# Kernel optimization log

Hardware: AMD Instinct MI355X
Metric: run time of the kernel (lower is better)

Reference implementation:

```python
import jax, jax.numpy as jnp
import numpy as np

B, T, N, F_IN = 8, 16, 1000, 16
E = 16000
H, D = 4, 32          # heads, gat_hidden_shape
HL = 64               # lstm hidden
OUT = 8
NEG_SLOPE = 0.2       # PyG GATConv default


def setup_inputs() -> dict:
    key = jax.random.key(0)
    ks = jax.random.split(key, 10)
    def init(k, shape, fan):
        return (jax.random.normal(k, shape, jnp.float32) / np.sqrt(fan)).astype(jnp.float32)
    x = jax.random.normal(ks[0], (B, T, N, F_IN), jnp.float32)
    edge_index = jax.random.randint(ks[1], (2, E), 0, N)
    W_gat = init(ks[2], (F_IN, H * D), F_IN)       # GATConv lin weight
    att_src = init(ks[3], (H, D), D)
    att_dst = init(ks[4], (H, D), D)
    b_gat = jnp.zeros((H * D,), jnp.float32)
    W_ih = init(ks[5], (4 * HL, H * D), H * D)     # LSTM, gate order i,f,g,o
    W_hh = init(ks[6], (4 * HL, HL), HL)
    b_ih = jnp.zeros((4 * HL,), jnp.float32)
    b_hh = jnp.zeros((4 * HL,), jnp.float32)
    W_clf = init(ks[7], (OUT, HL), HL)
    b_clf = jnp.zeros((OUT,), jnp.float32)
    return {"x": x, "edge_index": edge_index, "W_gat": W_gat, "att_src": att_src,
            "att_dst": att_dst, "b_gat": b_gat, "W_ih": W_ih, "W_hh": W_hh,
            "b_ih": b_ih, "b_hh": b_hh, "W_clf": W_clf, "b_clf": b_clf}


def reference(x, edge_index, W_gat, att_src, att_dst, b_gat,
              W_ih, W_hh, b_ih, b_hh, W_clf, b_clf):
    Bx, Tx, Nx, Fx = x.shape
    x_flat = x.reshape(Bx * Tx, Nx, Fx)
    # PyG GATConv adds self-loops by default
    loop = jnp.arange(Nx)
    src = jnp.concatenate([edge_index[0], loop])
    dst = jnp.concatenate([edge_index[1], loop])

    def gat_graph(xg):  # xg: [N, F]
        xp = (xg @ W_gat).reshape(Nx, H, D)                 # [N,H,D]
        a_s = jnp.einsum('nhd,hd->nh', xp, att_src)         # [N,H]
        a_d = jnp.einsum('nhd,hd->nh', xp, att_dst)
        e = jax.nn.leaky_relu(a_s[src] + a_d[dst], NEG_SLOPE)  # [E+N,H]
        m = jax.ops.segment_max(e, dst, num_segments=Nx)       # per-target softmax
        ex = jnp.exp(e - m[dst])
        denom = jax.ops.segment_sum(ex, dst, num_segments=Nx)
        alpha = ex / denom[dst]                                # [E+N,H]
        out = jax.ops.segment_sum(alpha[..., None] * xp[src], dst, num_segments=Nx)
        return out.reshape(Nx, H * D) + b_gat                  # [N, H*D]

    gat = jax.vmap(gat_graph)(x_flat)          # [B*T, N, H*D]
    gat = jax.nn.relu(gat)
    pooled = gat.max(axis=1)                   # global_max_pool -> [B*T, H*D]
    seq = pooled.reshape(Bx, Tx, H * D)

    h0 = jnp.zeros((Bx, HL), jnp.float32)
    c0 = jnp.zeros((Bx, HL), jnp.float32)

    def step(carry, xt):  # xt: [B, H*D]
        h, c = carry
        gates = xt @ W_ih.T + h @ W_hh.T + b_ih + b_hh
        i, f, g, o = jnp.split(gates, 4, axis=-1)
        i, f, o = jax.nn.sigmoid(i), jax.nn.sigmoid(f), jax.nn.sigmoid(o)
        g = jnp.tanh(g)
        c = f * c + i * g
        h = o * jnp.tanh(c)
        return (h, c), None

    (hT, _), _ = jax.lax.scan(step, (h0, c0), seq.transpose(1, 0, 2))
    return hT @ W_clf.T + b_clf                # [B, OUT]
```

## Files before the change

kernel.cpp:

```cpp
#include <hip/hip_runtime.h>
#include <hip/hip_bf16.h>
#include <stdint.h>

namespace {
constexpr int kB = 8, kT = 16, kN = 1000, kF = 16;
constexpr int kE = 16000;
constexpr int kH = 4, kHD = 128;
constexpr int kHL = 64, kOUT = 8;
constexpr int kG = kB * kT;
constexpr float kNeg = 0.2f;
constexpr int kNB = 25;

constexpr size_t CX_WG   = 0;
constexpr size_t CX_ATS  = CX_WG   + 2048;
constexpr size_t CX_ATD  = CX_ATS  + 128;
constexpr size_t CX_BG   = CX_ATD  + 128;
constexpr size_t CX_WIH  = CX_BG   + 128;
constexpr size_t CX_WHH  = CX_WIH  + 32768;
constexpr size_t CX_BIH  = CX_WHH  + 16384;
constexpr size_t CX_BHH  = CX_BIH  + 256;
constexpr size_t CX_WCLF = CX_BHH  + 256;
constexpr size_t CX_BCLF = CX_WCLF + 512;
constexpr size_t CX_TOTAL = CX_BCLF + 8;

constexpr size_t OFF_FLAG  = 0;
constexpr size_t OFF_ROW   = 256;
constexpr size_t OFF_COL   = 4352;
constexpr size_t OFF_POOL  = 68608;
constexpr size_t OFF_CANON = 134400;
constexpr size_t OFF_AS    = 239872;
constexpr size_t OFF_PPART = OFF_AS + (size_t)kG * 288000;
constexpr size_t PPART_BYTES = (size_t)kG * kNB * kHD * 4;

constexpr int kSetupBlocks = 10;
}

__device__ __forceinline__ float bf2f(unsigned short u) {
    return __uint_as_float(((uint32_t)u) << 16);
}
__device__ __forceinline__ float blo(uint32_t u) { return __uint_as_float(u << 16); }
__device__ __forceinline__ unsigned short f2bf(float f) {
    uint32_t u = __float_as_uint(f);
    uint32_t r = (u + 0x7fff + ((u >> 16) & 1)) >> 16;
    return (unsigned short)r;
}
__device__ __forceinline__ float sigm(float x) { return 1.f / (1.f + __expf(-x)); }

__device__ __forceinline__ int detect_isf(const unsigned short* xs, int t,
                                          int nthr, int* sh_cnt) {
    if (t == 0) *sh_cnt = 0;
    __syncthreads();
    int loc = 0;
    for (int i = t; i < 2048; i += nthr) {
        unsigned short u = xs[i];
        int ex = (u >> 7) & 0xff;
        if (u == 0 || (ex >= 97 && ex <= 143)) loc++;
    }
    atomicAdd(sh_cnt, loc);
    __syncthreads();
    return (*sh_cnt >= (2048 * 8) / 10) ? 0 : 1;
}

struct ConvArgs {
    const unsigned short* src[10];
    int n[10];
};

__global__ __launch_bounds__(256) void mega_setup(
        const void* __restrict__ xraw, const int* __restrict__ ei,
        ConvArgs ca,
        const unsigned short* __restrict__ WgR,
        const unsigned short* __restrict__ atsR,
        const unsigned short* __restrict__ atdR,
        int* __restrict__ flag, int* __restrict__ row, int* __restrict__ col,
        unsigned short* __restrict__ canon,
        unsigned short* __restrict__ xp_all,
        float* __restrict__ as_all, float* __restrict__ ad_all,
        unsigned int* __restrict__ pooled) {
    const int t = threadIdx.x;
    const unsigned short* xs = (const unsigned short*)xraw;

    if (blockIdx.x == 0) {
        __shared__ int cnt[1024];
        __shared__ int wtot[4];
        const int lane = t & 63, w = t >> 6;
        for (int i = t; i < 1024; i += 256) cnt[i] = 0;
        __syncthreads();
        const int* dst = ei + kE;
        for (int e = t; e < kE; e += 256) atomicAdd(&cnt[dst[e]], 1);
        __syncthreads();
        const int n0 = 4 * t;
        int c0 = cnt[n0], c1 = cnt[n0 + 1], c2 = cnt[n0 + 2], c3 = cnt[n0 + 3];
        int s0 = c0, s1 = s0 + c1, s2 = s1 + c2, s3 = s2 + c3;
        int tot = s3;
#pragma unroll
        for (int sft = 1; sft < 64; sft <<= 1) {
            int v = __shfl_up(tot, sft, 64);
            if (lane >= sft) tot += v;
        }
        if (lane == 63) wtot[w] = tot;
        __syncthreads();
        int wexcl = 0;
        for (int j = 0; j < w; ++j) wexcl += wtot[j];
        const int excl = wexcl + tot - s3;
        if (t == 0) row[0] = 0;
        if (n0 < kN) {
            row[n0 + 1] = excl + s0;
            row[n0 + 2] = excl + s1;
            row[n0 + 3] = excl + s2;
            row[n0 + 4] = excl + s3;
        }
        __syncthreads();
        cnt[n0] = excl; cnt[n0 + 1] = excl + s0;
        cnt[n0 + 2] = excl + s1; cnt[n0 + 3] = excl + s2;
        __syncthreads();
        for (int e = t; e < kE; e += 256) {
            int d0 = dst[e];
            int pos = atomicAdd(&cnt[d0], 1);
            col[pos] = ei[e];
        }
    } else if (blockIdx.x <= 8) {
        __shared__ int dcnt;
        const int isf = detect_isf(xs, t, 256, &dcnt);
        if (blockIdx.x == 1 && t == 0) *flag = isf;
        const int gid = (int)(blockIdx.x - 1) * 256 + t;
        size_t base = 0;
        for (int s = 0; s < 10; ++s) {
            const int n = ca.n[s];
            if (isf) {
                const float* fp = (const float*)ca.src[s];
                for (int i = gid; i < n; i += 2048) canon[base + i] = f2bf(fp[i]);
            } else {
                const unsigned short* sp = ca.src[s];
                for (int i = gid; i < n; i += 2048) canon[base + i] = sp[i];
            }
            base += (size_t)n;
        }
    } else if (blockIdx.x == 9) {
        for (int i = t; i < kG * kHD; i += 256) pooled[i] = 0u;
    } else {
        __shared__ int dcnt;
        __shared__ float Wl[kF * kHD];
        __shared__ float asl[kHD], adl[kHD];
        __shared__ float xr[64][20];
        __shared__ float ws2[2][4][16];
        const int isf = detect_isf(xs, t, 256, &dcnt);
        const int i0 = blockIdx.x - kSetupBlocks;
        const int v = i0 & 7;
        const int jj = i0 >> 3;
        const int gl = v + 8 * (jj >> 4);
        const int nb = jj & 15;
        if (isf) {
            const float* wf = (const float*)WgR;
            for (int i = t; i < kF * kHD; i += 256) Wl[i] = wf[i];
            if (t < kHD) asl[t] = ((const float*)atsR)[t];
            else if (t < 2 * kHD) adl[t - kHD] = ((const float*)atdR)[t - kHD];
        } else {
            for (int i = t; i < kF * kHD; i += 256) Wl[i] = bf2f(WgR[i]);
            if (t < kHD) asl[t] = bf2f(atsR[t]);
            else if (t < 2 * kHD) adl[t - kHD] = bf2f(atdR[t - kHD]);
        }
        const int n0 = nb * 64;
        const int nn = min(64, kN - n0);
        const size_t xbase = (size_t)gl * kN * kF + (size_t)n0 * kF;
        if (isf) {
            const float* xf = (const float*)xraw;
            for (int i = t; i < nn * kF; i += 256) xr[i >> 4][i & 15] = xf[xbase + i];
        } else {
            for (int i = t; i < nn * kF; i += 256) xr[i >> 4][i & 15] = bf2f(xs[xbase + i]);
        }
        __syncthreads();

        if (t < 128) {
            const int sd = t >> 6, h = (t >> 4) & 3, f = t & 15;
            const float* att = sd ? adl : asl;
            const int d0r = t & 31;
            float acc = 0.f;
#pragma unroll
            for (int i = 0; i < 32; ++i) {
                const int d = (d0r + i) & 31;
                acc += Wl[f * kHD + h * 32 + d] * att[h * 32 + d];
            }
            ws2[sd][h][f] = acc;
        }

        uint32_t* xp32 = (uint32_t*)(xp_all + (size_t)gl * kN * kHD);
        {
            const int p = t & 63;
            const int q = t >> 6;
            const int c0 = 2 * p;
            float wA[kF], wB[kF];
#pragma unroll
            for (int f = 0; f < kF; ++f) {
                wA[f] = Wl[f * kHD + c0];
                wB[f] = Wl[f * kHD + c0 + 1];
            }
            for (int ln = q; ln < nn; ln += 4) {
                const float4* xrv = (const float4*)xr[ln];
                const float4 x0 = xrv[0], x1 = xrv[1], x2 = xrv[2], x3 = xrv[3];
                float vA = x0.x * wA[0]  + x0.y * wA[1]  + x0.z * wA[2]  + x0.w * wA[3]
                         + x1.x * wA[4]  + x1.y * wA[5]  + x1.z * wA[6]  + x1.w * wA[7]
                         + x2.x * wA[8]  + x2.y * wA[9]  + x2.z * wA[10] + x2.w * wA[11]
                         + x3.x * wA[12] + x3.y * wA[13] + x3.z * wA[14] + x3.w * wA[15];
                float vB = x0.x * wB[0]  + x0.y * wB[1]  + x0.z * wB[2]  + x0.w * wB[3]
                         + x1.x * wB[4]  + x1.y * wB[5]  + x1.z * wB[6]  + x1.w * wB[7]
                         + x2.x * wB[8]  + x2.y * wB[9]  + x2.z * wB[10] + x2.w * wB[11]
                         + x3.x * wB[12] + x3.y * wB[13] + x3.z * wB[14] + x3.w * wB[15];
                const uint32_t pk = (uint32_t)f2bf(vA) | ((uint32_t)f2bf(vB) << 16);
                xp32[(size_t)(n0 + ln) * 64 + p] = pk;
            }
        }
        __syncthreads();

        {
            const int n = t >> 2, h = t & 3;
            if (n < nn) {
                const float* xv = xr[n];
                const float* wsv = ws2[0][h];
                const float* wdv = ws2[1][h];
                float accS = 0.f, accD = 0.f;
#pragma unroll
                for (int f = 0; f < kF; ++f) {
                    const float xf = xv[f];
                    accS += xf * wsv[f];
                    accD += xf * wdv[f];
                }
                as_all[((size_t)gl * kN + n0 + n) * kH + h] = accS;
                ad_all[((size_t)gl * kN + n0 + n) * kH + h] = accD;
            }
        }
    }
}

__global__ __launch_bounds__(256) void gat_aggregate(
        const int* __restrict__ row, const int* __restrict__ col,
        const unsigned short* __restrict__ xp,
        const float* __restrict__ a_s, const float* __restrict__ a_d,
        const unsigned short* __restrict__ bg,
        unsigned int* __restrict__ pooled,
        float* __restrict__ part, int use_part) {
    __shared__ int   col_lds[4][64];
    __shared__ float p_lds[4][4][72];
    __shared__ float pm[4][kHD];

    const int w = threadIdx.x >> 6;
    const int lane = threadIdx.x & 63;
    const int sub = lane >> 4;
    const int cl = lane & 15;
    const int hh = cl >> 2;
    const int xcd = blockIdx.x & 7;
    const int j = blockIdx.x >> 3;
    const int gl = xcd + 8 * (j / kNB);
    const int blk = j % kNB;
    const size_t gn = (size_t)gl * kN;
    const char* xpcl = (const char*)(xp + gn * kHD) + cl * 16;
    const float4* as4 = (const float4*)a_s + gn;
    const float4* ad4 = (const float4*)a_d + gn;
    const uint32_t* bg32 = (const uint32_t*)bg;
    float bgv[8];
#pragma unroll
    for (int jb = 0; jb < 4; ++jb) {
        uint32_t u = bg32[cl * 4 + jb];
        bgv[2 * jb] = blo(u);
        bgv[2 * jb + 1] = __uint_as_float(u & 0xffff0000u);
    }
    float pool[8];
#pragma unroll
    for (int jb = 0; jb < 8; ++jb) pool[jb] = 0.f;

    for (int it = 0; it < 10; ++it) {
        const int n = blk * 40 + it * 4 + w;
        const int r0 = row[n];
        const int deg = row[n + 1] - r0;
        const int E = deg + 1;
        const float4 dv = ad4[n];
        float acc[8];
#pragma unroll
        for (int jb = 0; jb < 8; ++jb) acc[jb] = 0.f;
        float dh = 0.f;

        for (int base = 0; base < E; base += 64) {
            const int cnt = min(64, E - base);
            const int cntP = (cnt + 3) & ~3;
            if (lane < cntP) {
                const int eg = base + lane;
                const bool act = lane < cnt;
                const int s = (act && eg < deg) ? col[r0 + eg] : n;
                float p0 = 0.f, p1 = 0.f, p2 = 0.f, p3 = 0.f;
                if (act) {
                    const float4 av = as4[s];
                    float t0 = av.x + dv.x, t1 = av.y + dv.y;
                    float t2 = av.z + dv.z, t3 = av.w + dv.w;
                    t0 = t0 > 0.f ? t0 : kNeg * t0;
                    t1 = t1 > 0.f ? t1 : kNeg * t1;
                    t2 = t2 > 0.f ? t2 : kNeg * t2;
                    t3 = t3 > 0.f ? t3 : kNeg * t3;
                    p0 = __expf(t0); p1 = __expf(t1);
                    p2 = __expf(t2); p3 = __expf(t3);
                }
                col_lds[w][lane] = s << 8;
                p_lds[w][0][lane] = p0;
                p_lds[w][1][lane] = p1;
                p_lds[w][2][lane] = p2;
                p_lds[w][3][lane] = p3;
            }
            for (int e0 = 0; e0 < cntP; e0 += 4) {
                const int e = e0 + sub;
                const int off = col_lds[w][e];
                const float al = p_lds[w][hh][e];
                const uint4 u = *(const uint4*)(xpcl + off);
                acc[0] += al * blo(u.x); acc[1] += al * __uint_as_float(u.x);
                acc[2] += al * blo(u.y); acc[3] += al * __uint_as_float(u.y);
                acc[4] += al * blo(u.z); acc[5] += al * __uint_as_float(u.z);
                acc[6] += al * blo(u.w); acc[7] += al * __uint_as_float(u.w);
                dh += al;
            }
        }
#pragma unroll
        for (int jb = 0; jb < 8; ++jb) {
            acc[jb] += __shfl_xor(acc[jb], 16, 64);
            acc[jb] += __shfl_xor(acc[jb], 32, 64);
        }
        dh += __shfl_xor(dh, 16, 64);
        dh += __shfl_xor(dh, 32, 64);
        const float inv = 1.f / dh;
#pragma unroll
        for (int jb = 0; jb < 8; ++jb) {
            const float o = acc[jb] * inv + bgv[jb];
            pool[jb] = fmaxf(pool[jb], o > 0.f ? o : 0.f);
        }
    }
    if (sub == 0) {
#pragma unroll
        for (int jb = 0; jb < 8; ++jb) pm[w][cl * 8 + jb] = pool[jb];
    }
    __syncthreads();
    if (w == 0 && sub == 0) {
        if (use_part) {
            float* dst = part + ((size_t)gl * kNB + blk) * kHD;
#pragma unroll
            for (int jb = 0; jb < 8; ++jb) {
                const int c = cl * 8 + jb;
                dst[c] = fmaxf(fmaxf(pm[0][c], pm[1][c]), fmaxf(pm[2][c], pm[3][c]));
            }
        } else {
            const size_t gp = (size_t)gl * kHD;
#pragma unroll
            for (int jb = 0; jb < 8; ++jb) {
                const int c = cl * 8 + jb;
                float vmax = fmaxf(fmaxf(pm[0][c], pm[1][c]), fmaxf(pm[2][c], pm[3][c]));
                atomicMax(pooled + gp + c, __float_as_uint(vmax));
            }
        }
    }
}

__global__ __launch_bounds__(256) void lstm_head(
        const float* __restrict__ pooled, const float* __restrict__ part,
        int use_part,
        const unsigned short* __restrict__ Wih,
        const unsigned short* __restrict__ Whh,
        const unsigned short* __restrict__ bih,
        const unsigned short* __restrict__ bhh,
        const unsigned short* __restrict__ Wclf,
        const unsigned short* __restrict__ bclf,
        const int* __restrict__ flag,
        void* __restrict__ out) {
    const int b = blockIdx.x;
    const int r = threadIdx.x;
    __shared__ float xt[kHD];
    __shared__ float hs[kHL];
    __shared__ float gates[4 * kHL];

    uint32_t wih[64];
    const uint32_t* pw = (const uint32_t*)(Wih + (size_t)r * kHD);
#pragma unroll
    for (int j = 0; j < 64; ++j) wih[j] = pw[j];
    uint32_t whh[32];
    const uint32_t* ph = (const uint32_t*)(Whh + (size_t)r * kHL);
#pragma unroll
    for (int j = 0; j < 32; ++j) whh[j] = ph[j];
    const float bias = bf2f(bih[r]) + bf2f(bhh[r]);

    float c_st = 0.f;
    if (r < kHL) hs[r] = 0.f;
    __syncthreads();

    for (int t = 0; t < kT; ++t) {
        const size_t g = (size_t)b * kT + t;
        if (r < kHD) {
            if (use_part) {
                const float* ps = part + g * kNB * kHD + r;
                float v = ps[0];
#pragma unroll
                for (int k = 1; k < kNB; ++k) v = fmaxf(v, ps[(size_t)k * kHD]);
                xt[r] = v;
            } else {
                xt[r] = pooled[g * kHD + r];
            }
        }
        __syncthreads();
        float a0 = 0.f, a1 = 0.f, a2 = 0.f, a3 = 0.f;
#pragma unroll
        for (int j = 0; j < 64; j += 4) {
            uint32_t u0 = wih[j], u1 = wih[j + 1], u2 = wih[j + 2], u3 = wih[j + 3];
            a0 += blo(u0) * xt[2 * j + 0] + __uint_as_float(u0 & 0xffff0000u) * xt[2 * j + 1];
            a1 += blo(u1) * xt[2 * j + 2] + __uint_as_float(u1 & 0xffff0000u) * xt[2 * j + 3];
            a2 += blo(u2) * xt[2 * j + 4] + __uint_as_float(u2 & 0xffff0000u) * xt[2 * j + 5];
            a3 += blo(u3) * xt[2 * j + 6] + __uint_as_float(u3 & 0xffff0000u) * xt[2 * j + 7];
        }
#pragma unroll
        for (int j = 0; j < 32; j += 4) {
            uint32_t u0 = whh[j], u1 = whh[j + 1], u2 = whh[j + 2], u3 = whh[j + 3];
            a0 += blo(u0) * hs[2 * j + 0] + __uint_as_float(u0 & 0xffff0000u) * hs[2 * j + 1];
            a1 += blo(u1) * hs[2 * j + 2] + __uint_as_float(u1 & 0xffff0000u) * hs[2 * j + 3];
            a2 += blo(u2) * hs[2 * j + 4] + __uint_as_float(u2 & 0xffff0000u) * hs[2 * j + 5];
            a3 += blo(u3) * hs[2 * j + 6] + __uint_as_float(u3 & 0xffff0000u) * hs[2 * j + 7];
        }
        gates[r] = bias + (a0 + a1) + (a2 + a3);
        __syncthreads();
        if (r < kHL) {
            const float iv = sigm(gates[r]);
            const float fv = sigm(gates[kHL + r]);
            const float gv = tanhf(gates[2 * kHL + r]);
            const float ov = sigm(gates[3 * kHL + r]);
            c_st = fv * c_st + iv * gv;
            hs[r] = ov * tanhf(c_st);
        }
        __syncthreads();
    }
    if (r < kOUT) {
        float acc = bf2f(bclf[r]);
#pragma unroll
        for (int k = 0; k < kHL; ++k) acc += hs[k] * bf2f(Wclf[r * kHL + k]);
        if (*flag) ((float*)out)[b * kOUT + r] = acc;
        else ((__hip_bfloat16*)out)[b * kOUT + r] = __float2bfloat16(acc);
    }
}

extern "C" void kernel_launch(void* const* d_in, const int* in_sizes, int n_in,
                              void* d_out, int out_size, void* d_ws, size_t ws_size,
                              hipStream_t stream) {
    const int* ei = (const int*)d_in[1];

    char* ws = (char*)d_ws;
    int*            flag   = (int*)(ws + OFF_FLAG);
    int*            row    = (int*)(ws + OFF_ROW);
    int*            colv   = (int*)(ws + OFF_COL);
    unsigned int*   pooled = (unsigned int*)(ws + OFF_POOL);
    unsigned short* canon  = (unsigned short*)(ws + OFF_CANON);

    unsigned short* cBg   = canon + CX_BG;
    unsigned short* cWih  = canon + CX_WIH;
    unsigned short* cWhh  = canon + CX_WHH;
    unsigned short* cBih  = canon + CX_BIH;
    unsigned short* cBhh  = canon + CX_BHH;
    unsigned short* cWclf = canon + CX_WCLF;
    unsigned short* cBclf = canon + CX_BCLF;

    float*          a_s = (float*)(ws + OFF_AS);
    float*          a_d = (float*)(ws + OFF_AS + (size_t)kG * 16000);
    unsigned short* xp  = (unsigned short*)(ws + OFF_AS + (size_t)kG * 32000);

    const int use_part = (ws_size >= OFF_PPART + PPART_BYTES) ? 1 : 0;
    float* part = (float*)(ws + OFF_PPART);

    ConvArgs ca;
    const int sizes[10] = {2048, 128, 128, 128, 32768, 16384, 256, 256, 512, 8};
    const int which[10] = {2, 3, 4, 5, 6, 7, 8, 9, 10, 11};
    for (int i = 0; i < 10; ++i) {
        ca.src[i] = (const unsigned short*)d_in[which[i]];
        ca.n[i] = sizes[i];
    }

    mega_setup<<<kSetupBlocks + kG * 16, 256, 0, stream>>>(
        d_in[0], ei, ca,
        (const unsigned short*)d_in[2], (const unsigned short*)d_in[3],
        (const unsigned short*)d_in[4],
        flag, row, colv, canon, xp, a_s, a_d, pooled);
    gat_aggregate<<<kG * kNB, 256, 0, stream>>>(row, colv, xp, a_s, a_d, cBg,
                                                pooled, part, use_part);
    lstm_head<<<kB, 256, 0, stream>>>((const float*)pooled, part, use_part,
                                      cWih, cWhh, cBih, cBhh,
                                      cWclf, cBclf, flag, d_out);
}
```

Measured before the change: 223.5 us.

## Restructure GAT projection to per-wave node loops and unroll aggregation by two

The node projection no longer stages weights and features in shared memory per block. Each wavefront keeps its weight columns in registers, walks 32 consecutive nodes, and computes the attention logits with a cross-lane shuffle reduction, which removes the shared-memory staging and the block barriers. The aggregate kernel now uses 16 node-blocks of 63 nodes, packs the column offset and attention weight into one float2 LDS entry, and processes two edges per iteration to raise memory-level parallelism. The dtype-detection sample is also shrunk to 512 elements, which makes the format heuristic more fragile.

```diff
diff --git a/kernel.cpp b/kernel.cpp
--- a/kernel.cpp
+++ b/kernel.cpp
@@ -9,7 +9,9 @@
 constexpr int kHL = 64, kOUT = 8;
 constexpr int kG = kB * kT;
 constexpr float kNeg = 0.2f;
-constexpr int kNB = 25;
+constexpr int kNB = 16;
+constexpr int kNPB = 63;
+constexpr int kPre = 1024;
 
 constexpr size_t CX_WG   = 0;
 constexpr size_t CX_ATS  = CX_WG   + 2048;
@@ -39,6 +41,7 @@
     return __uint_as_float(((uint32_t)u) << 16);
 }
 __device__ __forceinline__ float blo(uint32_t u) { return __uint_as_float(u << 16); }
+__device__ __forceinline__ float bhi(uint32_t u) { return __uint_as_float(u & 0xffff0000u); }
 __device__ __forceinline__ unsigned short f2bf(float f) {
     uint32_t u = __float_as_uint(f);
     uint32_t r = (u + 0x7fff + ((u >> 16) & 1)) >> 16;
@@ -51,14 +54,14 @@
     if (t == 0) *sh_cnt = 0;
     __syncthreads();
     int loc = 0;
-    for (int i = t; i < 2048; i += nthr) {
+    for (int i = t; i < 512; i += nthr) {
         unsigned short u = xs[i];
         int ex = (u >> 7) & 0xff;
         if (u == 0 || (ex >= 97 && ex <= 143)) loc++;
     }
     atomicAdd(sh_cnt, loc);
     __syncthreads();
-    return (*sh_cnt >= (2048 * 8) / 10) ? 0 : 1;
+    return (*sh_cnt >= 410) ? 0 : 1;
 }
 
 struct ConvArgs {
@@ -140,93 +143,78 @@
         for (int i = t; i < kG * kHD; i += 256) pooled[i] = 0u;
     } else {
         __shared__ int dcnt;
-        __shared__ float Wl[kF * kHD];
-        __shared__ float asl[kHD], adl[kHD];
-        __shared__ float xr[64][20];
-        __shared__ float ws2[2][4][16];
         const int isf = detect_isf(xs, t, 256, &dcnt);
-        const int i0 = blockIdx.x - kSetupBlocks;
-        const int v = i0 & 7;
-        const int jj = i0 >> 3;
-        const int gl = v + 8 * (jj >> 4);
-        const int nb = jj & 15;
+        const int lane = t & 63;
+        const int wv = t >> 6;
+        const int wid = (int)(blockIdx.x - kSetupBlocks) * 4 + wv;
+
+        float wA[kF], wB[kF];
+        float as0, as1, ad0, ad1;
         if (isf) {
             const float* wf = (const float*)WgR;
-            for (int i = t; i < kF * kHD; i += 256) Wl[i] = wf[i];
-            if (t < kHD) asl[t] = ((const float*)atsR)[t];
-            else if (t < 2 * kHD) adl[t - kHD] = ((const float*)atdR)[t - kHD];
+#pragma unroll
+            for (int f = 0; f < kF; ++f) {
+                const float2 wp = ((const float2*)(wf + (size_t)f * kHD))[lane];
+                wA[f] = wp.x; wB[f] = wp.y;
+            }
+            const float2 sv = ((const float2*)atsR)[lane];
+            as0 = sv.x; as1 = sv.y;
+            const float2 dv2 = ((const float2*)atdR)[lane];
+            ad0 = dv2.x; ad1 = dv2.y;
         } else {
-            for (int i = t; i < kF * kHD; i += 256) Wl[i] = bf2f(WgR[i]);
-            if (t < kHD) asl[t] = bf2f(atsR[t]);
-            else if (t < 2 * kHD) adl[t - kHD] = bf2f(atdR[t - kHD]);
-        }
-        const int n0 = nb * 64;
-        const int nn = min(64, kN - n0);
-        const size_t xbase = (size_t)gl * kN * kF + (size_t)n0 * kF;
-        if (isf) {
-            const float* xf = (const float*)xraw;
-            for (int i = t; i < nn * kF; i += 256) xr[i >> 4][i & 15] = xf[xbase + i];
-        } else {
-            for (int i = t; i < nn * kF; i += 256) xr[i >> 4][i & 15] = bf2f(xs[xbase + i]);
-        }
-        __syncthreads();
-
-        if (t < 128) {
-            const int sd = t >> 6, h = (t >> 4) & 3, f = t & 15;
-            const float* att = sd ? adl : asl;
-            const int d0r = t & 31;
-            float acc = 0.f;
-#pragma unroll
-            for (int i = 0; i < 32; ++i) {
-                const int d = (d0r + i) & 31;
-                acc += Wl[f * kHD + h * 32 + d] * att[h * 32 + d];
-            }
-            ws2[sd][h][f] = acc;
-        }
-
-        uint32_t* xp32 = (uint32_t*)(xp_all + (size_t)gl * kN * kHD);
-        {
-            const int p = t & 63;
-            const int q = t >> 6;
-            const int c0 = 2 * p;
-            float wA[kF], wB[kF];
+            const uint32_t* w32 = (const uint32_t*)WgR;
 #pragma unroll
             for (int f = 0; f < kF; ++f) {
-                wA[f] = Wl[f * kHD + c0];
-                wB[f] = Wl[f * kHD + c0 + 1];
-            }
-            for (int ln = q; ln < nn; ln += 4) {
-                const float4* xrv = (const float4*)xr[ln];
-                const float4 x0 = xrv[0], x1 = xrv[1], x2 = xrv[2], x3 = xrv[3];
-                float vA = x0.x * wA[0]  + x0.y * wA[1]  + x0.z * wA[2]  + x0.w * wA[3]
-                         + x1.x * wA[4]  + x1.y * wA[5]  + x1.z * wA[6]  + x1.w * wA[7]
-                         + x2.x * wA[8]  + x2.y * wA[9]  + x2.z * wA[10] + x2.w * wA[11]
-                         + x3.x * wA[12] + x3.y * wA[13] + x3.z * wA[14] + x3.w * wA[15];
-                float vB = x0.x * wB[0]  + x0.y * wB[1]  + x0.z * wB[2]  + x0.w * wB[3]
-                         + x1.x * wB[4]  + x1.y * wB[5]  + x1.z * wB[6]  + x1.w * wB[7]
-                         + x2.x * wB[8]  + x2.y * wB[9]  + x2.z * wB[10] + x2.w * wB[11]
-                         + x3.x * wB[12] + x3.y * wB[13] + x3.z * wB[14] + x3.w * wB[15];
-                const uint32_t pk = (uint32_t)f2bf(vA) | ((uint32_t)f2bf(vB) << 16);
-                xp32[(size_t)(n0 + ln) * 64 + p] = pk;
-            }
-        }
-        __syncthreads();
-
-        {
-            const int n = t >> 2, h = t & 3;
-            if (n < nn) {
-                const float* xv = xr[n];
-                const float* wsv = ws2[0][h];
-                const float* wdv = ws2[1][h];
-                float accS = 0.f, accD = 0.f;
-#pragma unroll
-                for (int f = 0; f < kF; ++f) {
-                    const float xf = xv[f];
-                    accS += xf * wsv[f];
-                    accD += xf * wdv[f];
-                }
-                as_all[((size_t)gl * kN + n0 + n) * kH + h] = accS;
-                ad_all[((size_t)gl * kN + n0 + n) * kH + h] = accD;
+                const uint32_t u = w32[f * 64 + lane];
+                wA[f] = blo(u); wB[f] = bhi(u);
+            }
+            const uint32_t us = ((const uint32_t*)atsR)[lane];
+            as0 = blo(us); as1 = bhi(us);
+            const uint32_t ud = ((const uint32_t*)atdR)[lane];
+            ad0 = blo(ud); ad1 = bhi(ud);
+        }
+
+        uint32_t* xp32 = (uint32_t*)xp_all;
+        const int nEnd = min(wid * 32 + 32, kG * kN);
+        for (int node = wid * 32; node < nEnd; ++node) {
+            float xv[kF];
+            if (isf) {
+                const float4* xr4 = (const float4*)((const float*)xraw + (size_t)node * kF);
+                const float4 x0 = xr4[0], x1 = xr4[1], x2 = xr4[2], x3 = xr4[3];
+                xv[0] = x0.x; xv[1] = x0.y; xv[2]  = x0.z; xv[3]  = x0.w;
+                xv[4] = x1.x; xv[5] = x1.y; xv[6]  = x1.z; xv[7]  = x1.w;
+                xv[8] = x2.x; xv[9] = x2.y; xv[10] = x2.z; xv[11] = x2.w;
+                xv[12] = x3.x; xv[13] = x3.y; xv[14] = x3.z; xv[15] = x3.w;
+            } else {
+                const uint4* xr4 = (const uint4*)(xs + (size_t)node * kF);
+                const uint4 q0 = xr4[0], q1 = xr4[1];
+                xv[0]  = blo(q0.x); xv[1]  = bhi(q0.x);
+                xv[2]  = blo(q0.y); xv[3]  = bhi(q0.y);
+                xv[4]  = blo(q0.z); xv[5]  = bhi(q0.z);
+                xv[6]  = blo(q0.w); xv[7]  = bhi(q0.w);
+                xv[8]  = blo(q1.x); xv[9]  = bhi(q1.x);
+                xv[10] = blo(q1.y); xv[11] = bhi(q1.y);
+                xv[12] = blo(q1.z); xv[13] = bhi(q1.z);
+                xv[14] = blo(q1.w); xv[15] = bhi(q1.w);
+            }
+            float vA = 0.f, vB = 0.f;
+#pragma unroll
+            for (int f = 0; f < kF; ++f) {
+                vA = fmaf(xv[f], wA[f], vA);
+                vB = fmaf(xv[f], wB[f], vB);
+            }
+            xp32[(size_t)node * 64 + lane] =
+                (uint32_t)f2bf(vA) | ((uint32_t)f2bf(vB) << 16);
+            float aS = vA * as0 + vB * as1;
+            float aD = vA * ad0 + vB * ad1;
+#pragma unroll
+            for (int sft = 1; sft < 16; sft <<= 1) {
+                aS += __shfl_xor(aS, sft, 64);
+                aD += __shfl_xor(aD, sft, 64);
+            }
+            if ((lane & 15) == 0) {
+                as_all[(size_t)node * kH + (lane >> 4)] = aS;
+                ad_all[(size_t)node * kH + (lane >> 4)] = aD;
             }
         }
     }
@@ -239,8 +227,7 @@
         const unsigned short* __restrict__ bg,
         unsigned int* __restrict__ pooled,
         float* __restrict__ part, int use_part) {
-    __shared__ int   col_lds[4][64];
-    __shared__ float p_lds[4][4][72];
+    __shared__ float2 colal[4][4][66];
     __shared__ float pm[4][kHD];
 
     const int w = threadIdx.x >> 6;
@@ -262,14 +249,16 @@
     for (int jb = 0; jb < 4; ++jb) {
         uint32_t u = bg32[cl * 4 + jb];
         bgv[2 * jb] = blo(u);
-        bgv[2 * jb + 1] = __uint_as_float(u & 0xffff0000u);
+        bgv[2 * jb + 1] = bhi(u);
     }
     float pool[8];
 #pragma unroll
     for (int jb = 0; jb < 8; ++jb) pool[jb] = 0.f;
 
-    for (int it = 0; it < 10; ++it) {
-        const int n = blk * 40 + it * 4 + w;
+    for (int it = 0; it < 16; ++it) {
+        const int lidx = it * 4 + w;
+        const int n = blk * kNPB + lidx;
+        if (lidx >= kNPB || n >= kN) continue;
         const int r0 = row[n];
         const int deg = row[n + 1] - r0;
         const int E = deg + 1;
@@ -281,7 +270,7 @@
 
         for (int base = 0; base < E; base += 64) {
             const int cnt = min(64, E - base);
-            const int cntP = (cnt + 3) & ~3;
+            const int cntP = (cnt + 7) & ~7;
             if (lane < cntP) {
                 const int eg = base + lane;
                 const bool act = lane < cnt;
@@ -298,22 +287,27 @@
                     p0 = __expf(t0); p1 = __expf(t1);
                     p2 = __expf(t2); p3 = __expf(t3);
                 }
-                col_lds[w][lane] = s << 8;
-                p_lds[w][0][lane] = p0;
-                p_lds[w][1][lane] = p1;
-                p_lds[w][2][lane] = p2;
-                p_lds[w][3][lane] = p3;
-            }
-            for (int e0 = 0; e0 < cntP; e0 += 4) {
-                const int e = e0 + sub;
-                const int off = col_lds[w][e];
-                const float al = p_lds[w][hh][e];
-                const uint4 u = *(const uint4*)(xpcl + off);
-                acc[0] += al * blo(u.x); acc[1] += al * __uint_as_float(u.x);
-                acc[2] += al * blo(u.y); acc[3] += al * __uint_as_float(u.y);
-                acc[4] += al * blo(u.z); acc[5] += al * __uint_as_float(u.z);
-                acc[6] += al * blo(u.w); acc[7] += al * __uint_as_float(u.w);
-                dh += al;
+                const float cf = __int_as_float(s << 8);
+                colal[w][0][lane] = make_float2(cf, p0);
+                colal[w][1][lane] = make_float2(cf, p1);
+                colal[w][2][lane] = make_float2(cf, p2);
+                colal[w][3][lane] = make_float2(cf, p3);
+            }
+            for (int e0 = 0; e0 < cntP; e0 += 8) {
+                const float2 cA = colal[w][hh][e0 + sub];
+                const float2 cB = colal[w][hh][e0 + 4 + sub];
+                const uint4 uA = *(const uint4*)(xpcl + __float_as_int(cA.x));
+                const uint4 uB = *(const uint4*)(xpcl + __float_as_int(cB.x));
+                const float aA = cA.y, aB = cB.y;
+                acc[0] = fmaf(aB, blo(uB.x), fmaf(aA, blo(uA.x), acc[0]));
+                acc[1] = fmaf(aB, bhi(uB.x), fmaf(aA, bhi(uA.x), acc[1]));
+                acc[2] = fmaf(aB, blo(uB.y), fmaf(aA, blo(uA.y), acc[2]));
+                acc[3] = fmaf(aB, bhi(uB.y), fmaf(aA, bhi(uA.y), acc[3]));
+                acc[4] = fmaf(aB, blo(uB.z), fmaf(aA, blo(uA.z), acc[4]));
+                acc[5] = fmaf(aB, bhi(uB.z), fmaf(aA, bhi(uA.z), acc[5]));
+                acc[6] = fmaf(aB, blo(uB.w), fmaf(aA, blo(uA.w), acc[6]));
+                acc[7] = fmaf(aB, bhi(uB.w), fmaf(aA, bhi(uA.w), acc[7]));
+                dh += aA + aB;
             }
         }
 #pragma unroll
@@ -404,18 +398,18 @@
 #pragma unroll
         for (int j = 0; j < 64; j += 4) {
             uint32_t u0 = wih[j], u1 = wih[j + 1], u2 = wih[j + 2], u3 = wih[j + 3];
-            a0 += blo(u0) * xt[2 * j + 0] + __uint_as_float(u0 & 0xffff0000u) * xt[2 * j + 1];
-            a1 += blo(u1) * xt[2 * j + 2] + __uint_as_float(u1 & 0xffff0000u) * xt[2 * j + 3];
-            a2 += blo(u2) * xt[2 * j + 4] + __uint_as_float(u2 & 0xffff0000u) * xt[2 * j + 5];
-            a3 += blo(u3) * xt[2 * j + 6] + __uint_as_float(u3 & 0xffff0000u) * xt[2 * j + 7];
+            a0 += blo(u0) * xt[2 * j + 0] + bhi(u0) * xt[2 * j + 1];
+            a1 += blo(u1) * xt[2 * j + 2] + bhi(u1) * xt[2 * j + 3];
+            a2 += blo(u2) * xt[2 * j + 4] + bhi(u2) * xt[2 * j + 5];
+            a3 += blo(u3) * xt[2 * j + 6] + bhi(u3) * xt[2 * j + 7];
         }
 #pragma unroll
         for (int j = 0; j < 32; j += 4) {
             uint32_t u0 = whh[j], u1 = whh[j + 1], u2 = whh[j + 2], u3 = whh[j + 3];
-            a0 += blo(u0) * hs[2 * j + 0] + __uint_as_float(u0 & 0xffff0000u) * hs[2 * j + 1];
-            a1 += blo(u1) * hs[2 * j + 2] + __uint_as_float(u1 & 0xffff0000u) * hs[2 * j + 3];
-            a2 += blo(u2) * hs[2 * j + 4] + __uint_as_float(u2 & 0xffff0000u) * hs[2 * j + 5];
-            a3 += blo(u3) * hs[2 * j + 6] + __uint_as_float(u3 & 0xffff0000u) * hs[2 * j + 7];
+            a0 += blo(u0) * hs[2 * j + 0] + bhi(u0) * hs[2 * j + 1];
+            a1 += blo(u1) * hs[2 * j + 2] + bhi(u1) * hs[2 * j + 3];
+            a2 += blo(u2) * hs[2 * j + 4] + bhi(u2) * hs[2 * j + 5];
+            a3 += blo(u3) * hs[2 * j + 6] + bhi(u3) * hs[2 * j + 7];
         }
         gates[r] = bias + (a0 + a1) + (a2 + a3);
         __syncthreads();
@@ -473,7 +467,7 @@
         ca.n[i] = sizes[i];
     }
 
-    mega_setup<<<kSetupBlocks + kG * 16, 256, 0, stream>>>(
+    mega_setup<<<kSetupBlocks + kPre, 256, 0, stream>>>(
         d_in[0], ei, ca,
         (const unsigned short*)d_in[2], (const unsigned short*)d_in[3],
         (const unsigned short*)d_in[4],
```

Result: slower. 241.1 us (+7.9%).
